# Kernel tuning notes

Hardware: AMD Instinct MI355X
Metric: run time of the kernel (lower is better)

The kernel has to match this reference:

```python
import jax, jax.numpy as jnp
import numpy as np

N = 50000      # n_nodes
E = 800000     # n_edges (nnz)
F = 256        # n_features
H = 256        # architecture (GCN hidden)
K = 16         # n_clusters
CLUSTER_REG = 1.0
CON_REG = 1.0


def setup_inputs() -> dict:
    key = jax.random.key(0)
    ks = jax.random.split(key, 12)
    inp = {
        "edge_src": jax.random.randint(ks[0], (E,), 0, N, dtype=jnp.int32),
        "edge_dst": jax.random.randint(ks[1], (E,), 0, N, dtype=jnp.int32),
        "edge_w_norm": jax.random.uniform(ks[2], (E,), dtype=jnp.float32),
        "features": jax.random.normal(ks[3], (N, F), dtype=jnp.float32),
        "aug_features": jax.random.normal(ks[4], (N, F), dtype=jnp.float32),
        # GCN encoder params (Linear no-bias + additive bias per DGI-style GCN)
        "W1": jax.random.normal(ks[5], (F, H), dtype=jnp.float32) / np.sqrt(F),
        "b1": jnp.zeros((H,), dtype=jnp.float32),
        # student GCN params
        "Ws": jax.random.normal(ks[6], (H, K), dtype=jnp.float32) / np.sqrt(H),
        "bs": jnp.zeros((K,), dtype=jnp.float32),
        # teacher GCN params (EMA copy; fixed here)
        "Wt": jax.random.normal(ks[7], (H, K), dtype=jnp.float32) / np.sqrt(H),
        "bt": jnp.zeros((K,), dtype=jnp.float32),
        "n_nodes": N,
    }
    return inp


def _spmm(w, src, dst, X, n):
    # (sparse A) @ X with A given as COO (src=row, dst=col, w=value)
    return jax.ops.segment_sum(w[:, None] * X[dst], src, num_segments=n)


def _gcn(X, W, b, w, src, dst, n):
    # act(spmm(A_norm, X @ W) + b) with act = selu
    return jax.nn.selu(_spmm(w, src, dst, X @ W, n) + b)


def _normalize(x):
    # F.normalize(x, dim=-1, p=2)
    nrm = jnp.sqrt(jnp.sum(x * x, axis=-1, keepdims=True))
    return x / jnp.maximum(nrm, 1e-12)


def reference(edge_src, edge_dst, edge_w_norm, features, aug_features,
              W1, b1, Ws, bs, Wt, bt, n_nodes):
    n = features.shape[0]
    n_edges = edge_src.shape[0]

    # encoder + student assignments
    gcn_out = _gcn(features, W1, b1, edge_w_norm, edge_src, edge_dst, n)
    logits = _spmm(edge_w_norm, edge_src, edge_dst, gcn_out @ Ws, n) + bs
    assignments = jax.nn.softmax(jax.nn.selu(logits), axis=1)  # [N, K]

    # degrees = torch.sparse.sum(graph, dim=0) (binary adjacency values)
    ones_e = jnp.ones((n_edges,), dtype=features.dtype)
    degrees = jax.ops.segment_sum(ones_e, edge_dst, num_segments=n)[:, None]  # [N,1]

    # graph_pooled = (A @ S).T @ S  (A values are all 1)
    AS = jax.ops.segment_sum(assignments[edge_dst], edge_src, num_segments=n)
    graph_pooled = AS.T @ assignments  # [K, K]

    normalizer_left = assignments.T @ degrees          # [K, 1]
    normalizer = (normalizer_left @ normalizer_left.T) / 2.0 / n_edges
    spectral_loss = -jnp.trace(graph_pooled - normalizer) / 2.0 / n_edges

    cluster_sizes = jnp.sum(assignments, axis=0)
    cluster_loss = (jnp.linalg.norm(cluster_sizes) / n_nodes * np.sqrt(float(K)) - 1.0)
    cluster_loss = cluster_loss * CLUSTER_REG

    # teacher branch (no grad)
    g2 = _gcn(aug_features, W1, b1, edge_w_norm, edge_src, edge_dst, n)
    t_logits = _spmm(edge_w_norm, edge_src, edge_dst, g2 @ Wt, n) + bt
    assignments_hat = jax.lax.stop_gradient(
        jax.nn.softmax(jax.nn.selu(t_logits), axis=-1))

    con = jnp.mean(2.0 - 2.0 * jnp.sum(_normalize(assignments_hat) * _normalize(assignments), axis=-1))

    loss = spectral_loss + cluster_loss + CON_REG * con
    return loss
```

## Files before the change

### kernel.cpp

```cpp
#include <hip/hip_runtime.h>
#include <math.h>

constexpr int Fdim = 256;
constexpr int Hdim = 256;
constexpr int Kc   = 16;

constexpr int RSTRIDE = 32;
constexpr int NRED    = 34;
constexpr int BCAP    = 5120;

typedef __attribute__((ext_vector_type(8))) short s8v;
typedef __attribute__((ext_vector_type(4))) float f4v;

__device__ __forceinline__ float selu1(float x){
    const float scale = 1.0507009873554805f;
    const float alpha = 1.6732632423543772f;
    return scale * (x > 0.f ? x : alpha * expm1f(x));
}

__device__ __forceinline__ ushort f2bf(float x){
    union { float f; unsigned u; } c; c.f = x;
    unsigned r = c.u + 0x7fffu + ((c.u >> 16) & 1u);
    return (ushort)(r >> 16);
}

__device__ __forceinline__ float bflo(unsigned v){
    union { unsigned u; float f; } c; c.u = v << 16; return c.f;
}
__device__ __forceinline__ float bfhi(unsigned v){
    union { unsigned u; float f; } c; c.u = v & 0xffff0000u; return c.f;
}

__device__ __forceinline__ unsigned char f2fp8(float x){
    int v = __builtin_amdgcn_cvt_pk_fp8_f32(x, x, 0, false);
    return (unsigned char)(v & 0xff);
}

__global__ __launch_bounds__(256) void bin_kernel(
        const int* __restrict__ src, const int* __restrict__ dst,
        const float* __restrict__ w,
        int* __restrict__ bcnt,
        int* __restrict__ bsrc, uint2* __restrict__ bdw, int E, int nbuck){
    __shared__ int hist[256];
    __shared__ int base[256];
    __shared__ int cur[256];
    int t = threadIdx.x;
    int chunk = (E + gridDim.x - 1) / gridDim.x;
    int lo = blockIdx.x * chunk;
    int hi = min(lo + chunk, E);
    hist[t] = 0;
    __syncthreads();
    for (int i = lo + t; i < hi; i += 256)
        atomicAdd(&hist[src[i] >> 8], 1);
    __syncthreads();
    if (t < nbuck && hist[t] > 0)
        base[t] = atomicAdd(&bcnt[t * 32], hist[t]);
    cur[t] = 0;
    __syncthreads();
    for (int i = lo + t; i < hi; i += 256){
        int s = src[i], d = dst[i];
        float wv = w[i];
        int b = s >> 8;
        int p = base[b] + atomicAdd(&cur[b], 1);
        if (p < BCAP){
            bsrc[(size_t)b * BCAP + p] = s;
            bdw[(size_t)b * BCAP + p]  = make_uint2((unsigned)d, __float_as_uint(wv));
        }
    }
}

__global__ __launch_bounds__(256) void bbase_kernel(const int* __restrict__ bcnt,
        int* __restrict__ bbase, int* __restrict__ roff, int nbuck, int n){
    __shared__ int s[256];
    int t = threadIdx.x;
    int v = (t < nbuck) ? min(bcnt[t * 32], BCAP) : 0;
    s[t] = v;
    __syncthreads();
    for (int off = 1; off < 256; off <<= 1){
        int x = (t >= off) ? s[t - off] : 0;
        __syncthreads();
        s[t] += x;
        __syncthreads();
    }
    if (t < nbuck) bbase[t] = s[t] - v;
    if (t == 255) roff[n] = s[255];
}

__global__ __launch_bounds__(256) void csr_build_kernel(
        const int* __restrict__ bcnt, const int* __restrict__ bbase,
        const int* __restrict__ bsrc, const uint2* __restrict__ bdw,
        int* __restrict__ roff, uint2* __restrict__ csr, int n){
    __shared__ int hist[256];
    __shared__ int loc[256];
    __shared__ int cur[256];
    int b = blockIdx.x, t = threadIdx.x;
    int cnt  = min(bcnt[b * 32], BCAP);
    int base = bbase[b];
    hist[t] = 0;
    __syncthreads();
    for (int i = t; i < cnt; i += 256)
        atomicAdd(&hist[bsrc[(size_t)b * BCAP + i] & 255], 1);
    __syncthreads();
    int v = hist[t];
    loc[t] = v;
    __syncthreads();
    for (int off = 1; off < 256; off <<= 1){
        int x = (t >= off) ? loc[t - off] : 0;
        __syncthreads();
        loc[t] += x;
        __syncthreads();
    }
    int gi = b * 256 + t;
    if (gi < n) roff[gi] = base + loc[t] - v;
    cur[t] = 0;
    __syncthreads();
    for (int i = t; i < cnt; i += 256){
        int s   = bsrc[(size_t)b * BCAP + i];
        int idx = s & 255;
        int p = base + (loc[idx] - hist[idx]) + atomicAdd(&cur[idx], 1);
        csr[p] = bdw[(size_t)b * BCAP + i];
    }
}

__global__ void castw_kernel(const float* __restrict__ W, ushort* __restrict__ Wt){
    __shared__ float t[16][17];
    int tx = threadIdx.x, ty = threadIdx.y;
    int k  = blockIdx.y * 16 + ty;
    int nn = blockIdx.x * 16 + tx;
    t[ty][tx] = W[k * 256 + nn];
    __syncthreads();
    int n2 = blockIdx.x * 16 + ty;
    int k2 = blockIdx.y * 16 + tx;
    Wt[n2 * 256 + k2] = f2bf(t[tx][ty]);
}

__global__ void castwk_kernel(const float* __restrict__ Ws, const float* __restrict__ Wt,
                              ushort* __restrict__ WsT, ushort* __restrict__ WtT){
    int h = threadIdx.x;
    #pragma unroll
    for (int c = 0; c < 16; ++c){
        WsT[c * 256 + h] = f2bf(Ws[h * 16 + c]);
        WtT[c * 256 + h] = f2bf(Wt[h * 16 + c]);
    }
}

__global__ __launch_bounds__(256, 2) void gemm_xw_kernel(
        const float* __restrict__ A0, const float* __restrict__ A1,
        const ushort* __restrict__ Bt,
        unsigned char* __restrict__ C8, int M){
    __shared__ ushort blds[32768];
    int tid = threadIdx.x;
    int n0  = blockIdx.x * 128;
    int bm  = blockIdx.y * 128;
    const float* A = blockIdx.z ? A1 : A0;
    int halfoff = blockIdx.z * 256;

    #pragma unroll
    for (int j = 0; j < 16; ++j){
        int c  = j * 256 + tid;
        int nl = c >> 5, kc = c & 31;
        uint4 v = *reinterpret_cast<const uint4*>(Bt + (((size_t)(n0 + nl)) << 8) + (kc << 3));
        unsigned boff = (unsigned)(((nl << 9) + (kc << 4)) ^ ((nl & 7) << 4));
        *reinterpret_cast<uint4*>(reinterpret_cast<char*>(blds) + boff) = v;
    }
    __syncthreads();

    int w = tid >> 6, l = tid & 63;
    int lr = l & 15, lk = l >> 4;

    f4v acc[2][8];
    #pragma unroll
    for (int m = 0; m < 2; ++m)
        #pragma unroll
        for (int t = 0; t < 8; ++t)
            acc[m][t] = (f4v){0.f, 0.f, 0.f, 0.f};

    int r0 = bm + w * 32 + lr;
    int r1 = r0 + 16;
    int rc0 = min(r0, M - 1), rc1 = min(r1, M - 1);
    const float* a0 = A + (size_t)rc0 * 256 + lk * 8;
    const float* a1 = A + (size_t)rc1 * 256 + lk * 8;

    for (int ks = 0; ks < 8; ++ks){
        s8v af0, af1;
        {
            float4 f0 = *reinterpret_cast<const float4*>(a0 + ks * 32);
            float4 f1 = *reinterpret_cast<const float4*>(a0 + ks * 32 + 4);
            af0[0] = (short)f2bf(f0.x); af0[1] = (short)f2bf(f0.y);
            af0[2] = (short)f2bf(f0.z); af0[3] = (short)f2bf(f0.w);
            af0[4] = (short)f2bf(f1.x); af0[5] = (short)f2bf(f1.y);
            af0[6] = (short)f2bf(f1.z); af0[7] = (short)f2bf(f1.w);
        }
        {
            float4 f0 = *reinterpret_cast<const float4*>(a1 + ks * 32);
            float4 f1 = *reinterpret_cast<const float4*>(a1 + ks * 32 + 4);
            af1[0] = (short)f2bf(f0.x); af1[1] = (short)f2bf(f0.y);
            af1[2] = (short)f2bf(f0.z); af1[3] = (short)f2bf(f0.w);
            af1[4] = (short)f2bf(f1.x); af1[5] = (short)f2bf(f1.y);
            af1[6] = (short)f2bf(f1.z); af1[7] = (short)f2bf(f1.w);
        }
        #pragma unroll
        for (int t = 0; t < 8; ++t){
            int nl = t * 16 + lr;
            unsigned boff = (unsigned)(((nl << 9) + ((ks * 4 + lk) << 4)) ^ ((nl & 7) << 4));
            s8v bf = *reinterpret_cast<const s8v*>(reinterpret_cast<const char*>(blds) + boff);
            acc[0][t] = __builtin_amdgcn_mfma_f32_16x16x32_bf16(af0, bf, acc[0][t], 0, 0, 0);
            acc[1][t] = __builtin_amdgcn_mfma_f32_16x16x32_bf16(af1, bf, acc[1][t], 0, 0, 0);
        }
    }

    #pragma unroll
    for (int m = 0; m < 2; ++m){
        #pragma unroll
        for (int t = 0; t < 8; ++t){
            int col = n0 + t * 16 + lr;
            #pragma unroll
            for (int j = 0; j < 4; ++j){
                int row = bm + w * 32 + m * 16 + lk * 4 + j;
                if (row < M) C8[(size_t)row * 512 + halfoff + col] = f2fp8(acc[m][t][j]);
            }
        }
    }
}

__global__ __launch_bounds__(256) void spmm_h2_kernel(
        const unsigned char* __restrict__ XWp,
        const int* __restrict__ roff, const uint2* __restrict__ csr,
        const float* __restrict__ b1,
        ushort* __restrict__ Gs, ushort* __restrict__ Gt, int n){
    int wid = threadIdx.x >> 6, lane = threadIdx.x & 63;
    int r = blockIdx.x * 4 + wid;
    if (r >= n) return;
    int half = lane >> 5;
    int hl   = lane & 31;
    const unsigned char* base = XWp + lane * 8;
    int e0 = roff[r], e1 = roff[r + 1];
    float acc[8] = {};

    #define ACCUM8(V, W) do{                                                      \
        auto fa_ = __builtin_amdgcn_cvt_pk_f32_fp8((V).x, false);                 \
        acc[0] = fmaf((W), fa_[0], acc[0]); acc[1] = fmaf((W), fa_[1], acc[1]);   \
        auto fb_ = __builtin_amdgcn_cvt_pk_f32_fp8((V).x, true);                  \
        acc[2] = fmaf((W), fb_[0], acc[2]); acc[3] = fmaf((W), fb_[1], acc[3]);   \
        auto fc_ = __builtin_amdgcn_cvt_pk_f32_fp8((V).y, false);                 \
        acc[4] = fmaf((W), fc_[0], acc[4]); acc[5] = fmaf((W), fc_[1], acc[5]);   \
        auto fd_ = __builtin_amdgcn_cvt_pk_f32_fp8((V).y, true);                  \
        acc[6] = fmaf((W), fd_[0], acc[6]); acc[7] = fmaf((W), fd_[1], acc[7]);   \
    }while(0)

    int e = e0;
    for (; e + 7 < e1; e += 8){
        uint2 c0 = csr[e],     c1 = csr[e + 1];
        uint2 c2 = csr[e + 2], c3 = csr[e + 3];
        uint2 c4 = csr[e + 4], c5 = csr[e + 5];
        uint2 c6 = csr[e + 6], c7 = csr[e + 7];
        uint2 v0 = *reinterpret_cast<const uint2*>(base + ((size_t)c0.x << 9));
        uint2 v1 = *reinterpret_cast<const uint2*>(base + ((size_t)c1.x << 9));
        uint2 v2 = *reinterpret_cast<const uint2*>(base + ((size_t)c2.x << 9));
        uint2 v3 = *reinterpret_cast<const uint2*>(base + ((size_t)c3.x << 9));
        uint2 v4 = *reinterpret_cast<const uint2*>(base + ((size_t)c4.x << 9));
        uint2 v5 = *reinterpret_cast<const uint2*>(base + ((size_t)c5.x << 9));
        uint2 v6 = *reinterpret_cast<const uint2*>(base + ((size_t)c6.x << 9));
        uint2 v7 = *reinterpret_cast<const uint2*>(base + ((size_t)c7.x << 9));
        ACCUM8(v0, __uint_as_float(c0.y)); ACCUM8(v1, __uint_as_float(c1.y));
        ACCUM8(v2, __uint_as_float(c2.y)); ACCUM8(v3, __uint_as_float(c3.y));
        ACCUM8(v4, __uint_as_float(c4.y)); ACCUM8(v5, __uint_as_float(c5.y));
        ACCUM8(v6, __uint_as_float(c6.y)); ACCUM8(v7, __uint_as_float(c7.y));
    }
    for (; e + 3 < e1; e += 4){
        uint2 c0 = csr[e],     c1 = csr[e + 1];
        uint2 c2 = csr[e + 2], c3 = csr[e + 3];
        uint2 v0 = *reinterpret_cast<const uint2*>(base + ((size_t)c0.x << 9));
        uint2 v1 = *reinterpret_cast<const uint2*>(base + ((size_t)c1.x << 9));
        uint2 v2 = *reinterpret_cast<const uint2*>(base + ((size_t)c2.x << 9));
        uint2 v3 = *reinterpret_cast<const uint2*>(base + ((size_t)c3.x << 9));
        ACCUM8(v0, __uint_as_float(c0.y)); ACCUM8(v1, __uint_as_float(c1.y));
        ACCUM8(v2, __uint_as_float(c2.y)); ACCUM8(v3, __uint_as_float(c3.y));
    }
    for (; e < e1; ++e){
        uint2 c = csr[e];
        uint2 v = *reinterpret_cast<const uint2*>(base + ((size_t)c.x << 9));
        ACCUM8(v, __uint_as_float(c.y));
    }
    #undef ACCUM8

    const float* bp = b1 + hl * 8;
    float4 bb0 = *reinterpret_cast<const float4*>(bp);
    float4 bb1 = *reinterpret_cast<const float4*>(bp + 4);
    float bv[8] = {bb0.x, bb0.y, bb0.z, bb0.w, bb1.x, bb1.y, bb1.z, bb1.w};
    ushort o[8];
    #pragma unroll
    for (int q = 0; q < 8; ++q) o[q] = f2bf(selu1(acc[q] + bv[q]));
    uint4 ov = *reinterpret_cast<const uint4*>(o);
    ushort* gout = (half ? Gt : Gs) + (size_t)r * Hdim + hl * 8;
    *reinterpret_cast<uint4*>(gout) = ov;
}

__global__ __launch_bounds__(256) void gemm_k2_kernel(
        const ushort* __restrict__ Gs, const ushort* __restrict__ Gt,
        const ushort* __restrict__ WsT, const ushort* __restrict__ WtT,
        unsigned* __restrict__ GSp, int n){
    int wv = blockIdx.x * 4 + (threadIdx.x >> 6);
    int l  = threadIdx.x & 63;
    int lr = l & 15, lk = l >> 4;
    int nw = (n + 15) >> 4;
    if (wv >= nw) return;
    int r0 = wv * 16;

    s8v bs_[8], bt_[8];
    #pragma unroll
    for (int ks = 0; ks < 8; ++ks){
        bs_[ks] = *reinterpret_cast<const s8v*>(WsT + lr * 256 + ks * 32 + lk * 8);
        bt_[ks] = *reinterpret_cast<const s8v*>(WtT + lr * 256 + ks * 32 + lk * 8);
    }

    f4v accs = (f4v){0.f,0.f,0.f,0.f}, acct = (f4v){0.f,0.f,0.f,0.f};
    int row = min(r0 + lr, n - 1);
    const ushort* gsrow = Gs + (size_t)row * 256 + lk * 8;
    const ushort* gtrow = Gt + (size_t)row * 256 + lk * 8;
    #pragma unroll
    for (int ks = 0; ks < 8; ++ks){
        s8v a_s = *reinterpret_cast<const s8v*>(gsrow + ks * 32);
        s8v a_t = *reinterpret_cast<const s8v*>(gtrow + ks * 32);
        accs = __builtin_amdgcn_mfma_f32_16x16x32_bf16(a_s, bs_[ks], accs, 0, 0, 0);
        acct = __builtin_amdgcn_mfma_f32_16x16x32_bf16(a_t, bt_[ks], acct, 0, 0, 0);
    }
    #pragma unroll
    for (int j = 0; j < 4; ++j){
        int rr = r0 + lk * 4 + j;
        if (rr < n){
            unsigned pv = (unsigned)f2bf(accs[j]) | ((unsigned)f2bf(acct[j]) << 16);
            GSp[(size_t)rr * 16 + lr] = pv;
        }
    }
}

__global__ __launch_bounds__(256) void spmm_k2_kernel(
        const unsigned* __restrict__ GSp,
        const int* __restrict__ roff, const uint2* __restrict__ csr,
        const float* __restrict__ bsv, const float* __restrict__ btv,
        float* __restrict__ asg, float* __restrict__ red, int n){
    int tid  = threadIdx.x;
    int wid  = tid >> 6, lane = tid & 63;
    int slot = lane >> 4, j = lane & 15;
    float bs_ = bsv[j], bt_ = btv[j];
    float cs_l = 0.f, con_l = 0.f;

    int rstride = gridDim.x * 4;
    for (int r = blockIdx.x * 4 + wid; r < n; r += rstride){
        int e0 = roff[r], e1 = roff[r + 1];
        float as_ = 0.f, at_ = 0.f;
        for (int e = e0 + slot; e < e1; e += 4){
            uint2 c = csr[e];
            float w = __uint_as_float(c.y);
            unsigned v = GSp[(size_t)c.x * 16 + j];
            as_ = fmaf(w, bflo(v), as_);
            at_ = fmaf(w, bfhi(v), at_);
        }
        as_ += __shfl_xor(as_, 16); as_ += __shfl_xor(as_, 32);
        at_ += __shfl_xor(at_, 16); at_ += __shfl_xor(at_, 32);
        float xs = selu1(as_ + bs_);
        float xt = selu1(at_ + bt_);
        float ms = xs, mt = xt;
        #pragma unroll
        for (int off = 8; off >= 1; off >>= 1){
            ms = fmaxf(ms, __shfl_xor(ms, off));
            mt = fmaxf(mt, __shfl_xor(mt, off));
        }
        float es = expf(xs - ms), et = expf(xt - mt);
        float ss = es, st = et;
        #pragma unroll
        for (int off = 8; off >= 1; off >>= 1){
            ss += __shfl_xor(ss, off);
            st += __shfl_xor(st, off);
        }
        float a = es / ss, b = et / st;
        if (slot == 0) asg[(size_t)r * 16 + j] = a;
        cs_l += a;
        float dot = a * b, na = a * a, nb = b * b;
        #pragma unroll
        for (int off = 8; off >= 1; off >>= 1){
            dot += __shfl_xor(dot, off);
            na  += __shfl_xor(na, off);
            nb  += __shfl_xor(nb, off);
        }
        if (j == 0){
            na = fmaxf(sqrtf(na), 1e-12f);
            nb = fmaxf(sqrtf(nb), 1e-12f);
            con_l += 2.f - 2.f * dot / (na * nb);
        }
    }

    cs_l  += __shfl_xor(cs_l, 16);  cs_l  += __shfl_xor(cs_l, 32);  cs_l  *= 0.25f;
    con_l += __shfl_xor(con_l, 16); con_l += __shfl_xor(con_l, 32); con_l *= 0.25f;

    __shared__ float part[4][17];
    if (lane < 16) part[wid][lane] = cs_l;
    if (lane == 0) part[wid][16]   = con_l;
    __syncthreads();
    if (tid < 16){
        float s = part[0][tid] + part[1][tid] + part[2][tid] + part[3][tid];
        atomicAdd(&red[(16 + tid) * RSTRIDE], s);
    } else if (tid == 16){
        float s = part[0][16] + part[1][16] + part[2][16] + part[3][16];
        atomicAdd(&red[32 * RSTRIDE], s);
    }
}

__global__ __launch_bounds__(256) void edge_trace_kernel(const int* __restrict__ src,
        const int* __restrict__ dst, const float* __restrict__ as_,
        float* __restrict__ red, int E){
    int tid    = blockIdx.x * blockDim.x + threadIdx.x;
    int stride = gridDim.x * blockDim.x;
    float dot = 0.f;
    float nl[16] = {};
    for (int i = tid; i < E; i += stride){
        const float4* pa = reinterpret_cast<const float4*>(as_ + (size_t)src[i] * 16);
        const float4* pb = reinterpret_cast<const float4*>(as_ + (size_t)dst[i] * 16);
        #pragma unroll
        for (int q = 0; q < 4; ++q){
            float4 va = pa[q]; float4 vb = pb[q];
            dot = fmaf(va.x, vb.x, dot); dot = fmaf(va.y, vb.y, dot);
            dot = fmaf(va.z, vb.z, dot); dot = fmaf(va.w, vb.w, dot);
            nl[q*4+0] += vb.x; nl[q*4+1] += vb.y;
            nl[q*4+2] += vb.z; nl[q*4+3] += vb.w;
        }
    }
    #pragma unroll
    for (int off = 1; off < 64; off <<= 1){
        dot += __shfl_xor(dot, off);
        #pragma unroll
        for (int k = 0; k < 16; ++k) nl[k] += __shfl_xor(nl[k], off);
    }
    __shared__ float part[4][17];
    int wid = threadIdx.x >> 6, lane = threadIdx.x & 63;
    if (lane == 0){
        #pragma unroll
        for (int k = 0; k < 16; ++k) part[wid][k] = nl[k];
        part[wid][16] = dot;
    }
    __syncthreads();
    int t = threadIdx.x;
    if (t < 16){
        float s = part[0][t] + part[1][t] + part[2][t] + part[3][t];
        atomicAdd(&red[t * RSTRIDE], s);
    } else if (t == 16){
        float s = part[0][16] + part[1][16] + part[2][16] + part[3][16];
        atomicAdd(&red[33 * RSTRIDE], s);
    }
}

__global__ void finalize_kernel(const float* __restrict__ red, float* __restrict__ out,
                                int n, int E){
    float trace = red[33 * RSTRIDE];
    float nl2 = 0.f, cs2 = 0.f;
    #pragma unroll
    for (int k = 0; k < 16; ++k){
        nl2 = fmaf(red[k * RSTRIDE],        red[k * RSTRIDE],        nl2);
        cs2 = fmaf(red[(16 + k) * RSTRIDE], red[(16 + k) * RSTRIDE], cs2);
    }
    float twoE = 2.f * (float)E;
    float spectral = -(trace - nl2 / twoE) / twoE;
    float cluster  = sqrtf(cs2) / (float)n * 4.f - 1.f;
    float con      = red[32 * RSTRIDE] / (float)n;
    out[0] = spectral + cluster + con;
}

extern "C" void kernel_launch(void* const* d_in, const int* in_sizes, int n_in,
                              void* d_out, int out_size, void* d_ws, size_t ws_size,
                              hipStream_t stream){
    const int*   esrc = (const int*)d_in[0];
    const int*   edst = (const int*)d_in[1];
    const float* ew   = (const float*)d_in[2];
    const float* feat = (const float*)d_in[3];
    const float* faug = (const float*)d_in[4];
    const float* W1   = (const float*)d_in[5];
    const float* b1   = (const float*)d_in[6];
    const float* Wsm  = (const float*)d_in[7];
    const float* bsv  = (const float*)d_in[8];
    const float* Wtm  = (const float*)d_in[9];
    const float* btv  = (const float*)d_in[10];
    int E = in_sizes[0];
    int N = in_sizes[3] / Fdim;

    char* ws = (char*)d_ws;
    size_t off = 0;
    auto alloc = [&](size_t bytes) -> char* {
        char* p = ws + off;
        off = (off + bytes + 255) & ~(size_t)255;
        return p;
    };
    int nbuck = (N + 255) >> 8;
    unsigned char* XWp = (unsigned char*)alloc((size_t)N * 512);
    ushort*   Gs    = (ushort*)alloc((size_t)N * Hdim * 2);
    ushort*   Gt    = (ushort*)alloc((size_t)N * Hdim * 2);
    unsigned* GSp   = (unsigned*)alloc((size_t)N * Kc * 4);
    float*    ASG_S = (float*)alloc((size_t)N * Kc * 4);
    ushort*   WT    = (ushort*)alloc((size_t)256 * 256 * 2);
    ushort*   WsT   = (ushort*)alloc((size_t)16 * 256 * 2);
    ushort*   WtT   = (ushort*)alloc((size_t)16 * 256 * 2);
    int*      ROFF  = (int*)alloc((size_t)(N + 1) * 4);
    int*      BBASE = (int*)alloc((size_t)(nbuck + 1) * 4);
    int*      BCNT  = (int*)alloc((size_t)nbuck * 32 * 4);
    int*      BSRC  = (int*)alloc((size_t)nbuck * BCAP * 4);
    uint2*    BDW   = (uint2*)alloc((size_t)nbuck * BCAP * 8);
    uint2*    CSR8  = (uint2*)alloc((size_t)E * 8);
    float*    RED   = (float*)alloc((size_t)NRED * RSTRIDE * 4);

    hipMemsetAsync(BCNT, 0, (size_t)nbuck * 32 * 4, stream);
    hipMemsetAsync(RED, 0, (size_t)NRED * RSTRIDE * 4, stream);

    castw_kernel<<<dim3(16, 16), dim3(16, 16), 0, stream>>>(W1, WT);
    castwk_kernel<<<1, 256, 0, stream>>>(Wsm, Wtm, WsT, WtT);
    bin_kernel<<<256, 256, 0, stream>>>(esrc, edst, ew, BCNT, BSRC, BDW, E, nbuck);
    bbase_kernel<<<1, 256, 0, stream>>>(BCNT, BBASE, ROFF, nbuck, N);
    csr_build_kernel<<<nbuck, 256, 0, stream>>>(BCNT, BBASE, BSRC, BDW, ROFF, CSR8, N);

    dim3 gg(2, (N + 127) / 128, 2);
    gemm_xw_kernel<<<gg, 256, 0, stream>>>(feat, faug, WT, XWp, N);

    spmm_h2_kernel<<<(N + 3) / 4, 256, 0, stream>>>(XWp, ROFF, CSR8, b1, Gs, Gt, N);

    int nw = (N + 15) / 16;
    gemm_k2_kernel<<<(nw + 3) / 4, 256, 0, stream>>>(Gs, Gt, WsT, WtT, GSp, N);

    spmm_k2_kernel<<<2048, 256, 0, stream>>>(GSp, ROFF, CSR8, bsv, btv,
                                             ASG_S, RED, N);

    edge_trace_kernel<<<256, 256, 0, stream>>>(esrc, edst, ASG_S, RED, E);
    finalize_kernel<<<1, 1, 0, stream>>>(RED, (float*)d_out, N, E);
}
```

Measured before the change: 248.2 us.

## Keep A fragments in registers and loop over both N halves per block

The XW GEMM previously launched separate blocks for each 128-column half of the output, so every block re-read and re-converted its 128 fp32 A rows to bf16. Now each block loads and converts its A rows once into registers (8 k-steps of fragments) and loops over both column halves, reloading only the B tile into LDS. This halves global reads of the large feature matrices and the conversion work. In exchange it raises register pressure (64 extra VGPRs of A fragments), halves the grid, and adds a second LDS fill plus an extra barrier per block.

New measurement: 254.8 us. 2.6% more time.

```diff
diff --git a/kernel.cpp b/kernel.cpp
--- a/kernel.cpp
+++ b/kernel.cpp
@@ -150,76 +150,79 @@
         unsigned char* __restrict__ C8, int M){
     __shared__ ushort blds[32768];
     int tid = threadIdx.x;
-    int n0  = blockIdx.x * 128;
-    int bm  = blockIdx.y * 128;
-    const float* A = blockIdx.z ? A1 : A0;
-    int halfoff = blockIdx.z * 256;
-
-    #pragma unroll
-    for (int j = 0; j < 16; ++j){
-        int c  = j * 256 + tid;
-        int nl = c >> 5, kc = c & 31;
-        uint4 v = *reinterpret_cast<const uint4*>(Bt + (((size_t)(n0 + nl)) << 8) + (kc << 3));
-        unsigned boff = (unsigned)(((nl << 9) + (kc << 4)) ^ ((nl & 7) << 4));
-        *reinterpret_cast<uint4*>(reinterpret_cast<char*>(blds) + boff) = v;
-    }
-    __syncthreads();
+    int bm  = blockIdx.x * 128;
+    const float* A = blockIdx.y ? A1 : A0;
+    int halfoff = blockIdx.y * 256;
 
     int w = tid >> 6, l = tid & 63;
     int lr = l & 15, lk = l >> 4;
-
-    f4v acc[2][8];
-    #pragma unroll
-    for (int m = 0; m < 2; ++m)
-        #pragma unroll
-        for (int t = 0; t < 8; ++t)
-            acc[m][t] = (f4v){0.f, 0.f, 0.f, 0.f};
 
     int r0 = bm + w * 32 + lr;
     int r1 = r0 + 16;
     int rc0 = min(r0, M - 1), rc1 = min(r1, M - 1);
     const float* a0 = A + (size_t)rc0 * 256 + lk * 8;
     const float* a1 = A + (size_t)rc1 * 256 + lk * 8;
-
+    s8v af0[8], af1[8];
+    #pragma unroll
     for (int ks = 0; ks < 8; ++ks){
-        s8v af0, af1;
-        {
-            float4 f0 = *reinterpret_cast<const float4*>(a0 + ks * 32);
-            float4 f1 = *reinterpret_cast<const float4*>(a0 + ks * 32 + 4);
-            af0[0] = (short)f2bf(f0.x); af0[1] = (short)f2bf(f0.y);
-            af0[2] = (short)f2bf(f0.z); af0[3] = (short)f2bf(f0.w);
-            af0[4] = (short)f2bf(f1.x); af0[5] = (short)f2bf(f1.y);
-            af0[6] = (short)f2bf(f1.z); af0[7] = (short)f2bf(f1.w);
-        }
-        {
-            float4 f0 = *reinterpret_cast<const float4*>(a1 + ks * 32);
-            float4 f1 = *reinterpret_cast<const float4*>(a1 + ks * 32 + 4);
-            af1[0] = (short)f2bf(f0.x); af1[1] = (short)f2bf(f0.y);
-            af1[2] = (short)f2bf(f0.z); af1[3] = (short)f2bf(f0.w);
-            af1[4] = (short)f2bf(f1.x); af1[5] = (short)f2bf(f1.y);
-            af1[6] = (short)f2bf(f1.z); af1[7] = (short)f2bf(f1.w);
-        }
-        #pragma unroll
-        for (int t = 0; t < 8; ++t){
-            int nl = t * 16 + lr;
-            unsigned boff = (unsigned)(((nl << 9) + ((ks * 4 + lk) << 4)) ^ ((nl & 7) << 4));
-            s8v bf = *reinterpret_cast<const s8v*>(reinterpret_cast<const char*>(blds) + boff);
-            acc[0][t] = __builtin_amdgcn_mfma_f32_16x16x32_bf16(af0, bf, acc[0][t], 0, 0, 0);
-            acc[1][t] = __builtin_amdgcn_mfma_f32_16x16x32_bf16(af1, bf, acc[1][t], 0, 0, 0);
-        }
-    }
-
-    #pragma unroll
-    for (int m = 0; m < 2; ++m){
-        #pragma unroll
-        for (int t = 0; t < 8; ++t){
-            int col = n0 + t * 16 + lr;
+        float4 f0 = *reinterpret_cast<const float4*>(a0 + ks * 32);
+        float4 f1 = *reinterpret_cast<const float4*>(a0 + ks * 32 + 4);
+        af0[ks][0] = (short)f2bf(f0.x); af0[ks][1] = (short)f2bf(f0.y);
+        af0[ks][2] = (short)f2bf(f0.z); af0[ks][3] = (short)f2bf(f0.w);
+        af0[ks][4] = (short)f2bf(f1.x); af0[ks][5] = (short)f2bf(f1.y);
+        af0[ks][6] = (short)f2bf(f1.z); af0[ks][7] = (short)f2bf(f1.w);
+        float4 g0 = *reinterpret_cast<const float4*>(a1 + ks * 32);
+        float4 g1 = *reinterpret_cast<const float4*>(a1 + ks * 32 + 4);
+        af1[ks][0] = (short)f2bf(g0.x); af1[ks][1] = (short)f2bf(g0.y);
+        af1[ks][2] = (short)f2bf(g0.z); af1[ks][3] = (short)f2bf(g0.w);
+        af1[ks][4] = (short)f2bf(g1.x); af1[ks][5] = (short)f2bf(g1.y);
+        af1[ks][6] = (short)f2bf(g1.z); af1[ks][7] = (short)f2bf(g1.w);
+    }
+
+    for (int h = 0; h < 2; ++h){
+        int n0 = h * 128;
+        #pragma unroll
+        for (int j = 0; j < 16; ++j){
+            int c  = j * 256 + tid;
+            int nl = c >> 5, kc = c & 31;
+            uint4 v = *reinterpret_cast<const uint4*>(Bt + (((size_t)(n0 + nl)) << 8) + (kc << 3));
+            unsigned boff = (unsigned)(((nl << 9) + (kc << 4)) ^ ((nl & 7) << 4));
+            *reinterpret_cast<uint4*>(reinterpret_cast<char*>(blds) + boff) = v;
+        }
+        __syncthreads();
+
+        f4v acc[2][8];
+        #pragma unroll
+        for (int m = 0; m < 2; ++m)
             #pragma unroll
-            for (int j = 0; j < 4; ++j){
-                int row = bm + w * 32 + m * 16 + lk * 4 + j;
-                if (row < M) C8[(size_t)row * 512 + halfoff + col] = f2fp8(acc[m][t][j]);
+            for (int t = 0; t < 8; ++t)
+                acc[m][t] = (f4v){0.f, 0.f, 0.f, 0.f};
+
+        #pragma unroll
+        for (int ks = 0; ks < 8; ++ks){
+            #pragma unroll
+            for (int t = 0; t < 8; ++t){
+                int nl = t * 16 + lr;
+                unsigned boff = (unsigned)(((nl << 9) + ((ks * 4 + lk) << 4)) ^ ((nl & 7) << 4));
+                s8v bf = *reinterpret_cast<const s8v*>(reinterpret_cast<const char*>(blds) + boff);
+                acc[0][t] = __builtin_amdgcn_mfma_f32_16x16x32_bf16(af0[ks], bf, acc[0][t], 0, 0, 0);
+                acc[1][t] = __builtin_amdgcn_mfma_f32_16x16x32_bf16(af1[ks], bf, acc[1][t], 0, 0, 0);
             }
         }
+
+        #pragma unroll
+        for (int m = 0; m < 2; ++m){
+            #pragma unroll
+            for (int t = 0; t < 8; ++t){
+                int col = n0 + t * 16 + lr;
+                #pragma unroll
+                for (int j = 0; j < 4; ++j){
+                    int row = bm + w * 32 + m * 16 + lk * 4 + j;
+                    if (row < M) C8[(size_t)row * 512 + halfoff + col] = f2fp8(acc[m][t][j]);
+                }
+            }
+        }
+        if (h == 0) __syncthreads();
     }
 }
 
@@ -516,7 +519,7 @@
     bbase_kernel<<<1, 256, 0, stream>>>(BCNT, BBASE, ROFF, nbuck, N);
     csr_build_kernel<<<nbuck, 256, 0, stream>>>(BCNT, BBASE, BSRC, BDW, ROFF, CSR8, N);
 
-    dim3 gg(2, (N + 127) / 128, 2);
+    dim3 gg((N + 127) / 128, 2);
     gemm_xw_kernel<<<gg, 256, 0, stream>>>(feat, faug, WT, XWp, N);
 
     spmm_h2_kernel<<<(N + 3) / 4, 256, 0, stream>>>(XWp, ROFF, CSR8, b1, Gs, Gt, N);
```
